# Optimization experiments

Measured on AMD Instinct MI355X. Metric: run time of the kernel, lower is better.

Reference implementation:

```python
import jax, jax.numpy as jnp
import numpy as np

B, S, D, H = 4, 2048, 1024, 16
HD = D // H


def setup_inputs() -> dict:
    key = jax.random.key(0)
    ks = jax.random.split(key, 12)
    inp = {
        "query": jax.random.normal(ks[0], (B, S, D), jnp.float32),
        "key": jax.random.normal(ks[1], (B, S, D), jnp.float32),
        "value": jax.random.normal(ks[2], (B, S, D), jnp.float32),
        "mask": jnp.tril(jnp.ones((S, S), jnp.int32)),  # causal mask
        "Wq": jax.random.normal(ks[3], (D, D), jnp.float32) / np.sqrt(D),
        "bq": jax.random.normal(ks[4], (D,), jnp.float32) * 0.02,
        "Wk": jax.random.normal(ks[5], (D, D), jnp.float32) / np.sqrt(D),
        "bk": jax.random.normal(ks[6], (D,), jnp.float32) * 0.02,
        "Wv": jax.random.normal(ks[7], (D, D), jnp.float32) / np.sqrt(D),
        "bv": jax.random.normal(ks[8], (D,), jnp.float32) * 0.02,
        "Wo": jax.random.normal(ks[9], (D, D), jnp.float32) / np.sqrt(D),
        "bo": jax.random.normal(ks[10], (D,), jnp.float32) * 0.02,
    }
    return inp


def reference(query, key, value, mask, Wq, bq, Wk, bk, Wv, bv, Wo, bo):
    # Linear projections (torch nn.Linear: y = x @ W.T + b)
    q = query @ Wq.T + bq
    k = key @ Wk.T + bk
    v = value @ Wv.T + bv
    # split heads: [B, S, D] -> [B, H, S, HD]
    q = q.reshape(B, S, H, HD).transpose(0, 2, 1, 3)
    k = k.reshape(B, S, H, HD).transpose(0, 2, 1, 3)
    v = v.reshape(B, S, H, HD).transpose(0, 2, 1, 3)
    # scaled dot-product attention with full [B,H,S,S] scores (faithful to source)
    scores = jnp.einsum("bhqd,bhkd->bhqk", q, k) / jnp.sqrt(jnp.float32(HD))
    scores = jnp.where(mask == 0, -jnp.inf, scores)
    attn = jax.nn.softmax(scores, axis=-1)
    out = jnp.einsum("bhqk,bhkd->bhqd", attn, v)
    # merge heads and output projection (dropout rate = 0.0 -> identity)
    out = out.transpose(0, 2, 1, 3).reshape(B, S, D)
    return out @ Wo.T + bo
```

## Files before the change

kernel.cpp:

```cpp
#include <hip/hip_runtime.h>

typedef __bf16 bf16x8 __attribute__((ext_vector_type(8)));
typedef __bf16 bf16x2 __attribute__((ext_vector_type(2)));
typedef float f32x4 __attribute__((ext_vector_type(4)));
typedef float f32x16 __attribute__((ext_vector_type(16)));
typedef unsigned short ushort;

__device__ __forceinline__ int4 cvt8(float4 a, float4 b) {
  bf16x8 v;
  v[0] = (__bf16)a.x; v[1] = (__bf16)a.y; v[2] = (__bf16)a.z; v[3] = (__bf16)a.w;
  v[4] = (__bf16)b.x; v[5] = (__bf16)b.y; v[6] = (__bf16)b.z; v[7] = (__bf16)b.w;
  return __builtin_bit_cast(int4, v);
}

__device__ __forceinline__ void gld16(const void* g, void* l) {
  __builtin_amdgcn_global_load_lds(
      (const __attribute__((address_space(1))) void*)g,
      (__attribute__((address_space(3))) void*)l, 16, 0, 0);
}

__device__ __forceinline__ unsigned pkbf(float a, float b) {
  bf16x2 v;
  v[0] = (__bf16)a;
  v[1] = (__bf16)b;
  return __builtin_bit_cast(unsigned, v);
}

#if __has_builtin(__builtin_amdgcn_permlane32_swap)
typedef unsigned u32x2 __attribute__((ext_vector_type(2)));
__device__ __forceinline__ void plswap(unsigned& a, unsigned& b, int hi) {
  (void)hi;
  u32x2 r = __builtin_amdgcn_permlane32_swap(a, b, false, false);
  a = r[0]; b = r[1];
}
#else
__device__ __forceinline__ void plswap(unsigned& a, unsigned& b, int hi) {
  const unsigned pa = (unsigned)__shfl_xor((int)a, 32);
  const unsigned pb = (unsigned)__shfl_xor((int)b, 32);
  const unsigned x = hi ? pb : a;
  const unsigned y = hi ? b : pa;
  a = x; b = y;
}
#endif

__device__ __forceinline__ f32x16 mfma32(bf16x8 a, bf16x8 b, f32x16 c) {
  return __builtin_amdgcn_mfma_f32_32x32x16_bf16(a, b, c, 0, 0, 0);
}

__global__ __launch_bounds__(256) void cvt4_k(const float* __restrict__ i0,
                                              const float* __restrict__ i1,
                                              const float* __restrict__ i2,
                                              const float* __restrict__ i3,
                                              ushort* __restrict__ o, int n8) {
  const int z = blockIdx.y;
  const float* in = (z == 0) ? i0 : (z == 1) ? i1 : (z == 2) ? i2 : i3;
  ushort* out = o + (size_t)z * 1024 * 1024;
  int i = blockIdx.x * 256 + threadIdx.x;
  if (i >= n8) return;
  const float4* p = (const float4*)in + (size_t)i * 2;
  *(int4*)(out + (size_t)i * 8) = cvt8(p[0], p[1]);
}

template <int AMODE, int WMODE, int OMODE>
__global__ __launch_bounds__(256) void gemm_k(const void* __restrict__ A,
                                              const void* __restrict__ W,
                                              const float* __restrict__ bias,
                                              void* __restrict__ Out,
                                              float oscale) {
  constexpr int K = 1024;
  __shared__ __align__(16) char lA[128 * 128];
  __shared__ __align__(16) char lB[128 * 128];
  const int t = threadIdx.x;
  const int l = t & 63;
  const int w = t >> 6;
  const int wr = w >> 1, wc = w & 1;
  const int m0 = blockIdx.x * 128;
  const int n0 = blockIdx.y * 128;
  const int srow = l >> 3;
  const int scol = ((l & 7) ^ srow) << 3;
  f32x4 acc[4][4];
#pragma unroll
  for (int i = 0; i < 4; ++i)
#pragma unroll
    for (int j = 0; j < 4; ++j) acc[i][j] = (f32x4){0.f, 0.f, 0.f, 0.f};

  for (int k0 = 0; k0 < K; k0 += 64) {
    if constexpr (AMODE == 1) {
#pragma unroll
      for (int i = 0; i < 4; ++i) {
        const int chunk = w * 4 + i;
        gld16((const ushort*)A + (size_t)(m0 + chunk * 8 + srow) * K + k0 + scol,
              lA + chunk * 1024);
      }
    } else {
#pragma unroll
      for (int qq = 0; qq < 4; ++qq) {
        const int L = t * 8 + qq * 2048;
        const int r = L >> 6, c = L & 63;
        const int dst = r * 128 + ((c * 2) ^ ((r & 7) << 4));
        const float* s0 = (const float*)A + (size_t)(m0 + r) * K + k0 + c;
        *(int4*)(lA + dst) = cvt8(*(const float4*)s0, *(const float4*)(s0 + 4));
      }
    }
    if constexpr (WMODE == 1) {
#pragma unroll
      for (int i = 0; i < 4; ++i) {
        const int chunk = w * 4 + i;
        gld16((const ushort*)W + (size_t)(n0 + chunk * 8 + srow) * K + k0 + scol,
              lB + chunk * 1024);
      }
    } else {
#pragma unroll
      for (int qq = 0; qq < 4; ++qq) {
        const int L = t * 8 + qq * 2048;
        const int r = L >> 6, c = L & 63;
        const int dst = r * 128 + ((c * 2) ^ ((r & 7) << 4));
        const float* s1 = (const float*)W + (size_t)(n0 + r) * K + k0 + c;
        *(int4*)(lB + dst) = cvt8(*(const float4*)s1, *(const float4*)(s1 + 4));
      }
    }
    __syncthreads();
#pragma unroll
    for (int ks = 0; ks < 2; ++ks) {
      const int kb = ks * 64 + ((l >> 4) << 4);
      bf16x8 af[4], bfv[4];
#pragma unroll
      for (int i = 0; i < 4; ++i) {
        const int row = wr * 64 + i * 16 + (l & 15);
        af[i] = *(const bf16x8*)(lA + row * 128 + (kb ^ ((row & 7) << 4)));
      }
#pragma unroll
      for (int j = 0; j < 4; ++j) {
        const int row = wc * 64 + j * 16 + (l & 15);
        bfv[j] = *(const bf16x8*)(lB + row * 128 + (kb ^ ((row & 7) << 4)));
      }
#pragma unroll
      for (int i = 0; i < 4; ++i)
#pragma unroll
        for (int j = 0; j < 4; ++j)
          acc[i][j] = __builtin_amdgcn_mfma_f32_16x16x32_bf16(af[i], bfv[j],
                                                              acc[i][j], 0, 0, 0);
    }
    __syncthreads();
  }
#pragma unroll
  for (int i = 0; i < 4; ++i)
#pragma unroll
    for (int j = 0; j < 4; ++j)
#pragma unroll
      for (int rg = 0; rg < 4; ++rg) {
        const int gm = m0 + wr * 64 + i * 16 + ((l >> 4) << 2) + rg;
        const int gn = n0 + wc * 64 + j * 16 + (l & 15);
        const float v = (acc[i][j][rg] + bias[gn]) * oscale;
        if constexpr (OMODE == 0) {
          const int b = gm >> 11, s = gm & 2047, h = gn >> 6, hd = gn & 63;
          ((ushort*)Out)[((((size_t)(b * 16 + h)) * 2048 + s) << 6) + hd] =
              __builtin_bit_cast(ushort, (__bf16)v);
        } else if constexpr (OMODE == 1) {
          const int b = gm >> 11, s = gm & 2047, h = gn >> 6, hd = gn & 63;
          ((ushort*)Out)[((((size_t)(b * 16 + h)) << 6) + hd) * 2048 + s] =
              __builtin_bit_cast(ushort, (__bf16)v);
        } else {
          ((float*)Out)[(size_t)gm * 1024 + gn] = v;
        }
      }
}

__global__ __launch_bounds__(256) void attn_k(const ushort* __restrict__ qh,
                                              const ushort* __restrict__ kh,
                                              const ushort* __restrict__ vth,
                                              ushort* __restrict__ out) {
  const int bh = blockIdx.x;
  const int qt = gridDim.y - 1 - blockIdx.y;
  const int q0 = qt * 128;
  const int t = threadIdx.x, l = t & 63, wv = t >> 6;
  const int lq = l & 31, hi = l >> 5;
  __shared__ __align__(16) char lk[2][64 * 128];
  __shared__ __align__(16) char lv[2][64 * 128];

  const int qrow = q0 + wv * 32 + lq;
  bf16x8 qf0, qf1, qf2, qf3;
  {
    const ushort* qp = qh + ((size_t)bh * 2048 + qrow) * 64 + hi * 8;
    qf0 = *(const bf16x8*)(qp);
    qf1 = *(const bf16x8*)(qp + 16);
    qf2 = *(const bf16x8*)(qp + 32);
    qf3 = *(const bf16x8*)(qp + 48);
  }
  bf16x8 ones8;
#pragma unroll
  for (int i = 0; i < 8; ++i) ones8[i] = (__bf16)1.0f;

  const int r0 = t >> 3;
  const int c0 = (t & 7) * 8;
  const ushort* kbase = kh + (size_t)bh * 2048 * 64 + (size_t)r0 * 64 + c0;
  const ushort* vbase = vth + (size_t)bh * 64 * 2048 + (size_t)r0 * 2048 + c0;
  const int dst0 = r0 * 128 + ((c0 * 2) ^ ((r0 & 7) << 4));

  int4 ka, kb2, va, vb2;
#define LOAD_TILE(kv0)                                            \
  do {                                                            \
    ka  = *(const int4*)(kbase + (size_t)(kv0) * 64);             \
    kb2 = *(const int4*)(kbase + (size_t)(kv0) * 64 + 32 * 64);   \
    va  = *(const int4*)(vbase + (kv0));                          \
    vb2 = *(const int4*)(vbase + (kv0) + 32 * 2048);              \
  } while (0)
#define WRITE_TILE(buf)                                           \
  do {                                                            \
    *(int4*)(lk[buf] + dst0) = ka;                                \
    *(int4*)(lk[buf] + dst0 + 32 * 128) = kb2;                    \
    *(int4*)(lv[buf] + dst0) = va;                                \
    *(int4*)(lv[buf] + dst0 + 32 * 128) = vb2;                    \
  } while (0)

  LOAD_TILE(0);
  WRITE_TILE(0);

  float m_r = -1e30f;
  f32x16 acco[2];
  f32x16 acc_l;
#pragma unroll
  for (int dt = 0; dt < 2; ++dt)
#pragma unroll
    for (int r = 0; r < 16; ++r) acco[dt][r] = 0.f;
#pragma unroll
  for (int r = 0; r < 16; ++r) acc_l[r] = 0.f;

  const int nt = 2 * qt + 2;
  int cur = 0;
#pragma unroll 1
  for (int ti = 0; ti < nt; ++ti) {
    __syncthreads();
    if (ti + 1 < nt) LOAD_TILE((ti + 1) << 6);

#pragma unroll
    for (int s = 0; s < 2; ++s) {
      const int kvs = (ti << 6) + s * 32;
      if (kvs > q0 + wv * 32 + 31) continue;

      f32x16 p;
#pragma unroll
      for (int r = 0; r < 16; ++r) p[r] = 0.f;
#pragma unroll
      for (int kd = 0; kd < 4; ++kd) {
        const int row = s * 32 + lq;
        const bf16x8 kf = *(const bf16x8*)(
            lk[cur] + row * 128 + ((kd * 32 + hi * 16) ^ ((row & 7) << 4)));
        const bf16x8 qf = (kd == 0) ? qf0 : (kd == 1) ? qf1 : (kd == 2) ? qf2 : qf3;
        p = mfma32(kf, qf, p);
      }
      if (kvs + 31 > q0 + wv * 32) {
#pragma unroll
        for (int r = 0; r < 16; ++r) {
          const int kv = kvs + (r & 3) + 8 * (r >> 2) + 4 * hi;
          if (kv > qrow) p[r] = -1e30f;
        }
      }
      const float a0 = fmaxf(fmaxf(p[0], p[1]), p[2]);
      const float a1 = fmaxf(fmaxf(p[3], p[4]), p[5]);
      const float a2 = fmaxf(fmaxf(p[6], p[7]), p[8]);
      const float a3 = fmaxf(fmaxf(p[9], p[10]), p[11]);
      const float a4 = fmaxf(fmaxf(p[12], p[13]), p[14]);
      const float b0 = fmaxf(fmaxf(a0, a1), a2);
      const float b1 = fmaxf(fmaxf(a3, a4), p[15]);
      float tm = fmaxf(b0, b1);
      tm = fmaxf(tm, __shfl_xor(tm, 32));
      if (!__all(tm <= m_r + 8.f)) {
        const float mn = fmaxf(m_r, tm);
        const float e = __builtin_amdgcn_exp2f(m_r - mn);
        m_r = mn;
#pragma unroll
        for (int dt = 0; dt < 2; ++dt)
#pragma unroll
          for (int r = 0; r < 16; ++r) acco[dt][r] *= e;
#pragma unroll
        for (int r = 0; r < 16; ++r) acc_l[r] *= e;
      }
#pragma unroll
      for (int r = 0; r < 16; ++r) p[r] = __builtin_amdgcn_exp2f(p[r] - m_r);
      unsigned W0a = pkbf(p[0], p[1]),   W0b = pkbf(p[2], p[3]);
      unsigned W1a = pkbf(p[4], p[5]),   W1b = pkbf(p[6], p[7]);
      unsigned W2a = pkbf(p[8], p[9]),   W2b = pkbf(p[10], p[11]);
      unsigned W3a = pkbf(p[12], p[13]), W3b = pkbf(p[14], p[15]);
#pragma unroll
      for (int ks = 0; ks < 2; ++ks) {
        unsigned a0u = ks ? W2a : W0a;
        unsigned a1u = ks ? W2b : W0b;
        unsigned b0u = ks ? W3a : W1a;
        unsigned b1u = ks ? W3b : W1b;
        plswap(a0u, b0u, hi);
        plswap(a1u, b1u, hi);
        const uint4 pw = {a0u, a1u, b0u, b1u};
        const bf16x8 pf = __builtin_bit_cast(bf16x8, pw);
        acc_l = mfma32(ones8, pf, acc_l);
#pragma unroll
        for (int dt = 0; dt < 2; ++dt) {
          const int row = dt * 32 + lq;
          const bf16x8 vf = *(const bf16x8*)(
              lv[cur] + row * 128 +
              ((s * 64 + ks * 32 + hi * 16) ^ ((row & 7) << 4)));
          acco[dt] = mfma32(vf, pf, acco[dt]);
        }
      }
    }
    if (ti + 1 < nt) WRITE_TILE(cur ^ 1);
    cur ^= 1;
  }
#undef LOAD_TILE
#undef WRITE_TILE
  const int b = bh >> 4, h = bh & 15;
  const float inv = __builtin_amdgcn_rcpf(acc_l[0]);
  ushort* orow = out + ((size_t)(b * 2048 + qrow)) * 1024 + h * 64;
#pragma unroll
  for (int dt = 0; dt < 2; ++dt)
#pragma unroll
    for (int g = 0; g < 4; ++g) {
      ushort4 st;
      st.x = __builtin_bit_cast(ushort, (__bf16)(acco[dt][4 * g + 0] * inv));
      st.y = __builtin_bit_cast(ushort, (__bf16)(acco[dt][4 * g + 1] * inv));
      st.z = __builtin_bit_cast(ushort, (__bf16)(acco[dt][4 * g + 2] * inv));
      st.w = __builtin_bit_cast(ushort, (__bf16)(acco[dt][4 * g + 3] * inv));
      *(ushort4*)(orow + dt * 32 + g * 8 + hi * 4) = st;
    }
}

extern "C" void kernel_launch(void* const* d_in, const int* in_sizes, int n_in,
                              void* d_out, int out_size, void* d_ws, size_t ws_size,
                              hipStream_t stream) {
  (void)in_sizes; (void)n_in; (void)out_size;
  const float* query = (const float*)d_in[0];
  const float* key = (const float*)d_in[1];
  const float* value = (const float*)d_in[2];
  const float* Wq = (const float*)d_in[4];
  const float* bq = (const float*)d_in[5];
  const float* Wk = (const float*)d_in[6];
  const float* bk = (const float*)d_in[7];
  const float* Wv = (const float*)d_in[8];
  const float* bv = (const float*)d_in[9];
  const float* Wo = (const float*)d_in[10];
  const float* bo = (const float*)d_in[11];

  char* ws = (char*)d_ws;
  const size_t SZA = (size_t)8192 * 1024 * 2;
  const size_t SZW = (size_t)1024 * 1024 * 2;
  ushort* qh = (ushort*)(ws + 0 * SZA);
  ushort* kh = (ushort*)(ws + 1 * SZA);
  ushort* vt = (ushort*)(ws + 2 * SZA);
  ushort* ao = (ushort*)(ws + 3 * SZA);
  dim3 bb(256), gg(64, 8), ga(64, 16);
  const float QS = 0.125f * 1.44269504088896f;

  if (ws_size >= 4 * SZA + 4 * SZW) {
    ushort* wq = (ushort*)(ws + 4 * SZA);
    ushort* wk = (ushort*)(ws + 4 * SZA + 1 * SZW);
    ushort* wv = (ushort*)(ws + 4 * SZA + 2 * SZW);
    ushort* wo = (ushort*)(ws + 4 * SZA + 3 * SZW);
    const int n8w = 1024 * 1024 / 8;
    hipLaunchKernelGGL(cvt4_k, dim3(n8w / 256, 4), bb, 0, stream, Wq, Wk, Wv, Wo, wq, n8w);
    hipLaunchKernelGGL((gemm_k<0, 1, 0>), gg, bb, 0, stream, (const void*)query, (const void*)wq, bq, (void*)qh, QS);
    hipLaunchKernelGGL((gemm_k<0, 1, 0>), gg, bb, 0, stream, (const void*)key, (const void*)wk, bk, (void*)kh, 1.0f);
    hipLaunchKernelGGL((gemm_k<0, 1, 1>), gg, bb, 0, stream, (const void*)value, (const void*)wv, bv, (void*)vt, 1.0f);
    hipLaunchKernelGGL(attn_k, ga, bb, 0, stream, qh, kh, vt, ao);
    hipLaunchKernelGGL((gemm_k<1, 1, 2>), gg, bb, 0, stream, (const void*)ao, (const void*)wo, bo, d_out, 1.0f);
  } else {
    hipLaunchKernelGGL((gemm_k<0, 0, 0>), gg, bb, 0, stream, (const void*)query, (const void*)Wq, bq, (void*)qh, QS);
    hipLaunchKernelGGL((gemm_k<0, 0, 0>), gg, bb, 0, stream, (const void*)key, (const void*)Wk, bk, (void*)kh, 1.0f);
    hipLaunchKernelGGL((gemm_k<0, 0, 1>), gg, bb, 0, stream, (const void*)value, (const void*)Wv, bv, (void*)vt, 1.0f);
    hipLaunchKernelGGL(attn_k, ga, bb, 0, stream, qh, kh, vt, ao);
    hipLaunchKernelGGL((gemm_k<1, 0, 2>), gg, bb, 0, stream, (const void*)ao, (const void*)Wo, bo, d_out, 1.0f);
  }
}
```

Measured before the change: 198.6 us.

## Pair causal query tiles per block and compute row sums with VALU

The attention kernel now uses 128-thread blocks over 64-row query tiles. Each block processes two tiles, a long one (31-y) and a short one (y), so causal work per block is balanced. The softmax denominator is now summed with VALU adds and a shuffle instead of an extra MFMA against a ones vector, which removes one MFMA per kv subtile. Smaller blocks carry fewer waves per block and have less K/V tile reuse across query rows, so global and LDS traffic per FLOP rises.

```diff
diff --git a/kernel.cpp b/kernel.cpp
--- a/kernel.cpp
+++ b/kernel.cpp
@@ -166,162 +166,181 @@
       }
 }
 
-__global__ __launch_bounds__(256) void attn_k(const ushort* __restrict__ qh,
+__global__ __launch_bounds__(128) void attn_k(const ushort* __restrict__ qh,
                                               const ushort* __restrict__ kh,
                                               const ushort* __restrict__ vth,
                                               ushort* __restrict__ out) {
   const int bh = blockIdx.x;
-  const int qt = gridDim.y - 1 - blockIdx.y;
-  const int q0 = qt * 128;
   const int t = threadIdx.x, l = t & 63, wv = t >> 6;
   const int lq = l & 31, hi = l >> 5;
   __shared__ __align__(16) char lk[2][64 * 128];
   __shared__ __align__(16) char lv[2][64 * 128];
 
-  const int qrow = q0 + wv * 32 + lq;
-  bf16x8 qf0, qf1, qf2, qf3;
-  {
-    const ushort* qp = qh + ((size_t)bh * 2048 + qrow) * 64 + hi * 8;
-    qf0 = *(const bf16x8*)(qp);
-    qf1 = *(const bf16x8*)(qp + 16);
-    qf2 = *(const bf16x8*)(qp + 32);
-    qf3 = *(const bf16x8*)(qp + 48);
-  }
-  bf16x8 ones8;
-#pragma unroll
-  for (int i = 0; i < 8; ++i) ones8[i] = (__bf16)1.0f;
-
-  const int r0 = t >> 3;
-  const int c0 = (t & 7) * 8;
-  const ushort* kbase = kh + (size_t)bh * 2048 * 64 + (size_t)r0 * 64 + c0;
-  const ushort* vbase = vth + (size_t)bh * 64 * 2048 + (size_t)r0 * 2048 + c0;
-  const int dst0 = r0 * 128 + ((c0 * 2) ^ ((r0 & 7) << 4));
-
-  int4 ka, kb2, va, vb2;
-#define LOAD_TILE(kv0)                                            \
-  do {                                                            \
-    ka  = *(const int4*)(kbase + (size_t)(kv0) * 64);             \
-    kb2 = *(const int4*)(kbase + (size_t)(kv0) * 64 + 32 * 64);   \
-    va  = *(const int4*)(vbase + (kv0));                          \
-    vb2 = *(const int4*)(vbase + (kv0) + 32 * 2048);              \
+  const int r0 = t >> 1;
+  const int cq = (t & 1) * 32;
+  const ushort* kbase = kh + (size_t)bh * 2048 * 64 + (size_t)r0 * 64 + cq;
+  const ushort* vbase = vth + (size_t)bh * 64 * 2048 + (size_t)r0 * 2048 + cq;
+  const int swz = (r0 & 7) << 4;
+  const int d0 = r0 * 128 + ((cq * 2 + 0) ^ swz);
+  const int d1 = r0 * 128 + ((cq * 2 + 16) ^ swz);
+  const int d2 = r0 * 128 + ((cq * 2 + 32) ^ swz);
+  const int d3 = r0 * 128 + ((cq * 2 + 48) ^ swz);
+  const int b = bh >> 4, h = bh & 15;
+
+  int4 ka0, ka1, ka2, ka3, va0, va1, va2, va3;
+#define LOAD_TILE(kv0)                                      \
+  do {                                                      \
+    const ushort* kp = kbase + (size_t)(kv0) * 64;          \
+    const ushort* vp = vbase + (kv0);                       \
+    ka0 = *(const int4*)(kp);                               \
+    ka1 = *(const int4*)(kp + 8);                           \
+    ka2 = *(const int4*)(kp + 16);                          \
+    ka3 = *(const int4*)(kp + 24);                          \
+    va0 = *(const int4*)(vp);                               \
+    va1 = *(const int4*)(vp + 8);                           \
+    va2 = *(const int4*)(vp + 16);                          \
+    va3 = *(const int4*)(vp + 24);                          \
   } while (0)
-#define WRITE_TILE(buf)                                           \
-  do {                                                            \
-    *(int4*)(lk[buf] + dst0) = ka;                                \
-    *(int4*)(lk[buf] + dst0 + 32 * 128) = kb2;                    \
-    *(int4*)(lv[buf] + dst0) = va;                                \
-    *(int4*)(lv[buf] + dst0 + 32 * 128) = vb2;                    \
+#define WRITE_TILE(buf)                                     \
+  do {                                                      \
+    *(int4*)(lk[buf] + d0) = ka0;                           \
+    *(int4*)(lk[buf] + d1) = ka1;                           \
+    *(int4*)(lk[buf] + d2) = ka2;                           \
+    *(int4*)(lk[buf] + d3) = ka3;                           \
+    *(int4*)(lv[buf] + d0) = va0;                           \
+    *(int4*)(lv[buf] + d1) = va1;                           \
+    *(int4*)(lv[buf] + d2) = va2;                           \
+    *(int4*)(lv[buf] + d3) = va3;                           \
   } while (0)
 
-  LOAD_TILE(0);
-  WRITE_TILE(0);
-
-  float m_r = -1e30f;
-  f32x16 acco[2];
-  f32x16 acc_l;
-#pragma unroll
-  for (int dt = 0; dt < 2; ++dt)
-#pragma unroll
-    for (int r = 0; r < 16; ++r) acco[dt][r] = 0.f;
-#pragma unroll
-  for (int r = 0; r < 16; ++r) acc_l[r] = 0.f;
-
-  const int nt = 2 * qt + 2;
-  int cur = 0;
 #pragma unroll 1
-  for (int ti = 0; ti < nt; ++ti) {
+  for (int pass = 0; pass < 2; ++pass) {
+    const int qt = pass ? blockIdx.y : (31 - blockIdx.y);
+    const int q0 = qt * 64;
+    const int qwave = q0 + wv * 32;
+    const int qrow = qwave + lq;
+
+    bf16x8 qf0, qf1, qf2, qf3;
+    {
+      const ushort* qp = qh + ((size_t)bh * 2048 + qrow) * 64 + hi * 8;
+      qf0 = *(const bf16x8*)(qp);
+      qf1 = *(const bf16x8*)(qp + 16);
+      qf2 = *(const bf16x8*)(qp + 32);
+      qf3 = *(const bf16x8*)(qp + 48);
+    }
+    LOAD_TILE(0);
     __syncthreads();
-    if (ti + 1 < nt) LOAD_TILE((ti + 1) << 6);
-
-#pragma unroll
-    for (int s = 0; s < 2; ++s) {
-      const int kvs = (ti << 6) + s * 32;
-      if (kvs > q0 + wv * 32 + 31) continue;
-
-      f32x16 p;
-#pragma unroll
-      for (int r = 0; r < 16; ++r) p[r] = 0.f;
-#pragma unroll
-      for (int kd = 0; kd < 4; ++kd) {
-        const int row = s * 32 + lq;
-        const bf16x8 kf = *(const bf16x8*)(
-            lk[cur] + row * 128 + ((kd * 32 + hi * 16) ^ ((row & 7) << 4)));
-        const bf16x8 qf = (kd == 0) ? qf0 : (kd == 1) ? qf1 : (kd == 2) ? qf2 : qf3;
-        p = mfma32(kf, qf, p);
-      }
-      if (kvs + 31 > q0 + wv * 32) {
-#pragma unroll
-        for (int r = 0; r < 16; ++r) {
-          const int kv = kvs + (r & 3) + 8 * (r >> 2) + 4 * hi;
-          if (kv > qrow) p[r] = -1e30f;
-        }
-      }
-      const float a0 = fmaxf(fmaxf(p[0], p[1]), p[2]);
-      const float a1 = fmaxf(fmaxf(p[3], p[4]), p[5]);
-      const float a2 = fmaxf(fmaxf(p[6], p[7]), p[8]);
-      const float a3 = fmaxf(fmaxf(p[9], p[10]), p[11]);
-      const float a4 = fmaxf(fmaxf(p[12], p[13]), p[14]);
-      const float b0 = fmaxf(fmaxf(a0, a1), a2);
-      const float b1 = fmaxf(fmaxf(a3, a4), p[15]);
-      float tm = fmaxf(b0, b1);
-      tm = fmaxf(tm, __shfl_xor(tm, 32));
-      if (!__all(tm <= m_r + 8.f)) {
-        const float mn = fmaxf(m_r, tm);
-        const float e = __builtin_amdgcn_exp2f(m_r - mn);
-        m_r = mn;
-#pragma unroll
-        for (int dt = 0; dt < 2; ++dt)
-#pragma unroll
-          for (int r = 0; r < 16; ++r) acco[dt][r] *= e;
-#pragma unroll
-        for (int r = 0; r < 16; ++r) acc_l[r] *= e;
-      }
-#pragma unroll
-      for (int r = 0; r < 16; ++r) p[r] = __builtin_amdgcn_exp2f(p[r] - m_r);
-      unsigned W0a = pkbf(p[0], p[1]),   W0b = pkbf(p[2], p[3]);
-      unsigned W1a = pkbf(p[4], p[5]),   W1b = pkbf(p[6], p[7]);
-      unsigned W2a = pkbf(p[8], p[9]),   W2b = pkbf(p[10], p[11]);
-      unsigned W3a = pkbf(p[12], p[13]), W3b = pkbf(p[14], p[15]);
-#pragma unroll
-      for (int ks = 0; ks < 2; ++ks) {
-        unsigned a0u = ks ? W2a : W0a;
-        unsigned a1u = ks ? W2b : W0b;
-        unsigned b0u = ks ? W3a : W1a;
-        unsigned b1u = ks ? W3b : W1b;
-        plswap(a0u, b0u, hi);
-        plswap(a1u, b1u, hi);
-        const uint4 pw = {a0u, a1u, b0u, b1u};
-        const bf16x8 pf = __builtin_bit_cast(bf16x8, pw);
-        acc_l = mfma32(ones8, pf, acc_l);
-#pragma unroll
-        for (int dt = 0; dt < 2; ++dt) {
-          const int row = dt * 32 + lq;
-          const bf16x8 vf = *(const bf16x8*)(
-              lv[cur] + row * 128 +
-              ((s * 64 + ks * 32 + hi * 16) ^ ((row & 7) << 4)));
-          acco[dt] = mfma32(vf, pf, acco[dt]);
-        }
-      }
-    }
-    if (ti + 1 < nt) WRITE_TILE(cur ^ 1);
-    cur ^= 1;
+    WRITE_TILE(0);
+
+    float m_r = -1e30f, l_r = 0.f;
+    f32x16 acco[2];
+#pragma unroll
+    for (int dt = 0; dt < 2; ++dt)
+#pragma unroll
+      for (int r = 0; r < 16; ++r) acco[dt][r] = 0.f;
+
+    const int nt = qt + 1;
+    int cur = 0;
+#pragma unroll 1
+    for (int ti = 0; ti < nt; ++ti) {
+      __syncthreads();
+      if (ti + 1 < nt) LOAD_TILE((ti + 1) << 6);
+
+#pragma unroll
+      for (int s = 0; s < 2; ++s) {
+        const int kvs = (ti << 6) + s * 32;
+        if (kvs > qwave + 31) continue;
+
+        f32x16 p;
+#pragma unroll
+        for (int r = 0; r < 16; ++r) p[r] = 0.f;
+#pragma unroll
+        for (int kd = 0; kd < 4; ++kd) {
+          const int row = s * 32 + lq;
+          const bf16x8 kf = *(const bf16x8*)(
+              lk[cur] + row * 128 + ((kd * 32 + hi * 16) ^ ((row & 7) << 4)));
+          const bf16x8 qf = (kd == 0) ? qf0 : (kd == 1) ? qf1 : (kd == 2) ? qf2 : qf3;
+          p = mfma32(kf, qf, p);
+        }
+        if (kvs + 31 > qwave) {
+#pragma unroll
+          for (int r = 0; r < 16; ++r) {
+            const int kv = kvs + (r & 3) + 8 * (r >> 2) + 4 * hi;
+            if (kv > qrow) p[r] = -1e30f;
+          }
+        }
+        const float a0 = fmaxf(fmaxf(p[0], p[1]), p[2]);
+        const float a1 = fmaxf(fmaxf(p[3], p[4]), p[5]);
+        const float a2 = fmaxf(fmaxf(p[6], p[7]), p[8]);
+        const float a3 = fmaxf(fmaxf(p[9], p[10]), p[11]);
+        const float a4 = fmaxf(fmaxf(p[12], p[13]), p[14]);
+        const float b0 = fmaxf(fmaxf(a0, a1), a2);
+        const float b1 = fmaxf(fmaxf(a3, a4), p[15]);
+        float tm = fmaxf(b0, b1);
+        tm = fmaxf(tm, __shfl_xor(tm, 32));
+        if (!__all(tm <= m_r + 8.f)) {
+          const float mn = fmaxf(m_r, tm);
+          const float e = __builtin_amdgcn_exp2f(m_r - mn);
+          m_r = mn;
+          l_r *= e;
+#pragma unroll
+          for (int dt = 0; dt < 2; ++dt)
+#pragma unroll
+            for (int r = 0; r < 16; ++r) acco[dt][r] *= e;
+        }
+#pragma unroll
+        for (int r = 0; r < 16; ++r) p[r] = __builtin_amdgcn_exp2f(p[r] - m_r);
+        float sr[8];
+#pragma unroll
+        for (int r = 0; r < 8; ++r) sr[r] = p[r] + p[r + 8];
+#pragma unroll
+        for (int r = 0; r < 4; ++r) sr[r] = sr[r] + sr[r + 4];
+        float rs = (sr[0] + sr[1]) + (sr[2] + sr[3]);
+        rs += __shfl_xor(rs, 32);
+        l_r += rs;
+        unsigned W0a = pkbf(p[0], p[1]),   W0b = pkbf(p[2], p[3]);
+        unsigned W1a = pkbf(p[4], p[5]),   W1b = pkbf(p[6], p[7]);
+        unsigned W2a = pkbf(p[8], p[9]),   W2b = pkbf(p[10], p[11]);
+        unsigned W3a = pkbf(p[12], p[13]), W3b = pkbf(p[14], p[15]);
+#pragma unroll
+        for (int ks = 0; ks < 2; ++ks) {
+          unsigned a0u = ks ? W2a : W0a;
+          unsigned a1u = ks ? W2b : W0b;
+          unsigned b0u = ks ? W3a : W1a;
+          unsigned b1u = ks ? W3b : W1b;
+          plswap(a0u, b0u, hi);
+          plswap(a1u, b1u, hi);
+          const uint4 pw = {a0u, a1u, b0u, b1u};
+          const bf16x8 pf = __builtin_bit_cast(bf16x8, pw);
+#pragma unroll
+          for (int dt = 0; dt < 2; ++dt) {
+            const int row = dt * 32 + lq;
+            const bf16x8 vf = *(const bf16x8*)(
+                lv[cur] + row * 128 +
+                ((s * 64 + ks * 32 + hi * 16) ^ ((row & 7) << 4)));
+            acco[dt] = mfma32(vf, pf, acco[dt]);
+          }
+        }
+      }
+      if (ti + 1 < nt) WRITE_TILE(cur ^ 1);
+      cur ^= 1;
+    }
+    const float inv = __builtin_amdgcn_rcpf(l_r);
+    ushort* orow = out + ((size_t)(b * 2048 + qrow)) * 1024 + h * 64;
+#pragma unroll
+    for (int dt = 0; dt < 2; ++dt)
+#pragma unroll
+      for (int g = 0; g < 4; ++g) {
+        ushort4 st;
+        st.x = __builtin_bit_cast(ushort, (__bf16)(acco[dt][4 * g + 0] * inv));
+        st.y = __builtin_bit_cast(ushort, (__bf16)(acco[dt][4 * g + 1] * inv));
+        st.z = __builtin_bit_cast(ushort, (__bf16)(acco[dt][4 * g + 2] * inv));
+        st.w = __builtin_bit_cast(ushort, (__bf16)(acco[dt][4 * g + 3] * inv));
+        *(ushort4*)(orow + dt * 32 + g * 8 + hi * 4) = st;
+      }
   }
 #undef LOAD_TILE
 #undef WRITE_TILE
-  const int b = bh >> 4, h = bh & 15;
-  const float inv = __builtin_amdgcn_rcpf(acc_l[0]);
-  ushort* orow = out + ((size_t)(b * 2048 + qrow)) * 1024 + h * 64;
-#pragma unroll
-  for (int dt = 0; dt < 2; ++dt)
-#pragma unroll
-    for (int g = 0; g < 4; ++g) {
-      ushort4 st;
-      st.x = __builtin_bit_cast(ushort, (__bf16)(acco[dt][4 * g + 0] * inv));
-      st.y = __builtin_bit_cast(ushort, (__bf16)(acco[dt][4 * g + 1] * inv));
-      st.z = __builtin_bit_cast(ushort, (__bf16)(acco[dt][4 * g + 2] * inv));
-      st.w = __builtin_bit_cast(ushort, (__bf16)(acco[dt][4 * g + 3] * inv));
-      *(ushort4*)(orow + dt * 32 + g * 8 + hi * 4) = st;
-    }
 }
 
 extern "C" void kernel_launch(void* const* d_in, const int* in_sizes, int n_in,
@@ -347,7 +366,7 @@
   ushort* kh = (ushort*)(ws + 1 * SZA);
   ushort* vt = (ushort*)(ws + 2 * SZA);
   ushort* ao = (ushort*)(ws + 3 * SZA);
-  dim3 bb(256), gg(64, 8), ga(64, 16);
+  dim3 bb(256), gg(64, 8), ga(64, 16), ba(128);
   const float QS = 0.125f * 1.44269504088896f;
 
   if (ws_size >= 4 * SZA + 4 * SZW) {
@@ -360,13 +379,13 @@
     hipLaunchKernelGGL((gemm_k<0, 1, 0>), gg, bb, 0, stream, (const void*)query, (const void*)wq, bq, (void*)qh, QS);
     hipLaunchKernelGGL((gemm_k<0, 1, 0>), gg, bb, 0, stream, (const void*)key, (const void*)wk, bk, (void*)kh, 1.0f);
     hipLaunchKernelGGL((gemm_k<0, 1, 1>), gg, bb, 0, stream, (const void*)value, (const void*)wv, bv, (void*)vt, 1.0f);
-    hipLaunchKernelGGL(attn_k, ga, bb, 0, stream, qh, kh, vt, ao);
+    hipLaunchKernelGGL(attn_k, ga, ba, 0, stream, qh, kh, vt, ao);
     hipLaunchKernelGGL((gemm_k<1, 1, 2>), gg, bb, 0, stream, (const void*)ao, (const void*)wo, bo, d_out, 1.0f);
   } else {
     hipLaunchKernelGGL((gemm_k<0, 0, 0>), gg, bb, 0, stream, (const void*)query, (const void*)Wq, bq, (void*)qh, QS);
     hipLaunchKernelGGL((gemm_k<0, 0, 0>), gg, bb, 0, stream, (const void*)key, (const void*)Wk, bk, (void*)kh, 1.0f);
     hipLaunchKernelGGL((gemm_k<0, 0, 1>), gg, bb, 0, stream, (const void*)value, (const void*)Wv, bv, (void*)vt, 1.0f);
-    hipLaunchKernelGGL(attn_k, ga, bb, 0, stream, qh, kh, vt, ao);
+    hipLaunchKernelGGL(attn_k, ga, ba, 0, stream, qh, kh, vt, ao);
     hipLaunchKernelGGL((gemm_k<1, 0, 2>), gg, bb, 0, stream, (const void*)ao, (const void*)Wo, bo, d_out, 1.0f);
   }
 }
```

After: 202.2 us. About the same (+1.8%).
